# Kernel tuning notes

Measured on AMD Instinct MI355X. Metric: run time of the kernel, lower is better.

Reference implementation:

```python
import jax, jax.numpy as jnp
import numpy as np

B, T, D = 2, 2048, 1024
NH = 16
HD = D // NH


def setup_inputs() -> dict:
    key = jax.random.key(0)
    ks = jax.random.split(key, 5)
    s = 0.02
    return {
        "x": jax.random.normal(ks[0], (B, T, D), dtype=jnp.float32),
        "Wq": jax.random.normal(ks[1], (D, D), dtype=jnp.float32) * s,
        "Wk": jax.random.normal(ks[2], (D, D), dtype=jnp.float32) * s,
        "Wv": jax.random.normal(ks[3], (D, D), dtype=jnp.float32) * s,
        "Wo": jax.random.normal(ks[4], (D, D), dtype=jnp.float32) * s,
        "bo": jnp.zeros((D,), dtype=jnp.float32),
    }


def reference(x, Wq, Wk, Wv, Wo, bo):
    b, t, _ = x.shape
    scale = HD ** -0.5
    # torch Linear: y = x @ W^T
    q = (x @ Wq.T).reshape(b, t, NH, HD)
    k = (x @ Wk.T).reshape(b, t, NH, HD)
    v = (x @ Wv.T).reshape(b, t, NH, HD)
    # scores: [b, nh, t, t]
    s = jnp.einsum("bqhd,bkhd->bhqk", q, k) * scale
    causal = jnp.tril(jnp.ones((t, t), dtype=bool))
    s = jnp.where(causal, s, -jnp.inf)
    p = jax.nn.softmax(s, axis=-1)
    o = jnp.einsum("bhqk,bkhd->bqhd", p, v).reshape(b, t, D)
    return o @ Wo.T + bo
```

## Files before the change

### kernel.cpp

```cpp
#include <hip/hip_runtime.h>


typedef __bf16 bf16x8 __attribute__((ext_vector_type(8)));
typedef float f32x4 __attribute__((ext_vector_type(4)));
typedef unsigned short ushortx8 __attribute__((ext_vector_type(8)));
typedef unsigned short ushortx4 __attribute__((ext_vector_type(4)));

#define T_SEQ 2048
#define NHEAD 16
#define HDIM 64
#define DMODEL 1024

__device__ inline unsigned short f2bf(float f) {
  unsigned int u = __builtin_bit_cast(unsigned int, f);
  unsigned int r = (u + 0x7fffu + ((u >> 16) & 1u)) >> 16;
  return (unsigned short)r;
}

__device__ inline void gl16(const unsigned short* g, unsigned short* l) {
  __builtin_amdgcn_global_load_lds(
      (const __attribute__((address_space(1))) unsigned int*)g,
      (__attribute__((address_space(3))) unsigned int*)l, 16, 0, 0);
}

__global__ void cast_all(const float* __restrict__ x, const float* __restrict__ w0,
                         const float* __restrict__ w1, const float* __restrict__ w2,
                         const float* __restrict__ w3, unsigned short* __restrict__ out) {
  const int NX = 2 * T_SEQ * DMODEL;
  int i = (blockIdx.x * 256 + threadIdx.x) * 4;
  const float* src;
  int off;
  if (i < NX) {
    src = x; off = i;
  } else {
    const int j = i - NX;
    const int sel = j >> 20;
    off = j & ((1 << 20) - 1);
    src = sel == 0 ? w0 : sel == 1 ? w1 : sel == 2 ? w2 : w3;
  }
  float4 v = *reinterpret_cast<const float4*>(src + off);
  ushortx4 o;
  o[0] = f2bf(v.x); o[1] = f2bf(v.y); o[2] = f2bf(v.z); o[3] = f2bf(v.w);
  *reinterpret_cast<ushortx4*>(out + i) = o;
}

__device__ __forceinline__ void gemm_core(
    const unsigned short* __restrict__ A, const unsigned short* __restrict__ Bw,
    int K, int m0, int n0, f32x4 acc[4][4]) {
  __shared__ unsigned short As[4096];
  __shared__ unsigned short Bs[4096];
  const int tid = threadIdx.x;
  const int lane = tid & 63, wid = tid >> 6;
  const int wr = wid >> 1, wc = wid & 1;
  const int lr = lane & 15, lg = lane >> 4;
  const int srow = tid >> 2;
  const int scs = ((tid & 3) ^ (srow & 3)) * 8;
  const unsigned short* ga0 = A + (size_t)(m0 + srow) * K + scs;
  const unsigned short* gb0 = Bw + (size_t)(n0 + srow) * K + scs;
  unsigned short* la0 = As + tid * 8;
  unsigned short* lb0 = Bs + tid * 8;
  const int rca = (lg ^ (lr & 3)) * 8;

  for (int k0 = 0; k0 < K; k0 += 32) {
    __syncthreads();
    gl16(ga0 + k0, la0);
    gl16(ga0 + (size_t)64 * K + k0, la0 + 2048);
    gl16(gb0 + k0, lb0);
    gl16(gb0 + (size_t)64 * K + k0, lb0 + 2048);
    __syncthreads();

    bf16x8 af[4], bfr[4];
#pragma unroll
    for (int t = 0; t < 4; ++t) {
      af[t]  = *reinterpret_cast<const bf16x8*>(&As[(wr * 64 + t * 16 + lr) * 32 + rca]);
      bfr[t] = *reinterpret_cast<const bf16x8*>(&Bs[(wc * 64 + t * 16 + lr) * 32 + rca]);
    }
#pragma unroll
    for (int mi = 0; mi < 4; ++mi)
#pragma unroll
      for (int ni = 0; ni < 4; ++ni)
        acc[mi][ni] = __builtin_amdgcn_mfma_f32_16x16x32_bf16(af[mi], bfr[ni], acc[mi][ni], 0, 0, 0);
  }
}

__global__ __launch_bounds__(256) void gemm_qkv(
    const unsigned short* __restrict__ xb, const unsigned short* __restrict__ Wall,
    unsigned short* __restrict__ Qb, unsigned short* __restrict__ Kb,
    unsigned short* __restrict__ Vtb) {
  const int z = blockIdx.y;
  const int bid = blockIdx.x;
  int m0, n0;
  const unsigned short* A;
  const unsigned short* Bw;
  if (z < 2) {
    n0 = (bid & 7) * 128; m0 = (bid >> 3) * 128;
    A = xb; Bw = Wall + (size_t)z * (DMODEL * DMODEL);
  } else {
    m0 = (bid & 7) * 128; n0 = (bid >> 3) * 128;
    A = Wall + (size_t)2 * (DMODEL * DMODEL); Bw = xb;
  }
  f32x4 acc[4][4] = {};
  gemm_core(A, Bw, DMODEL, m0, n0, acc);

  const int tid = threadIdx.x, lane = tid & 63, wid = tid >> 6;
  const int wr = wid >> 1, wc = wid & 1, lr = lane & 15, lg = lane >> 4;
  const int mb = m0 + wr * 64, nb = n0 + wc * 64;
  const float scale = z == 0 ? 0.125f * 1.44269504089f : 1.0f;
#pragma unroll
  for (int mi = 0; mi < 4; ++mi)
#pragma unroll
    for (int ni = 0; ni < 4; ++ni) {
      const int col = nb + ni * 16 + lr;
#pragma unroll
      for (int j = 0; j < 4; ++j) {
        const int row = mb + mi * 16 + lg * 4 + j;
        const float v = acc[mi][ni][j] * scale;
        if (z < 2) {
          const int b = row >> 11, t = row & (T_SEQ - 1);
          const int h = col >> 6, d = col & (HDIM - 1);
          unsigned short* out = z == 0 ? Qb : Kb;
          out[(((size_t)(b * NHEAD + h) * T_SEQ + t) << 6) + d] = f2bf(v);
        } else {
          const int h = row >> 6, d = row & (HDIM - 1);
          const int b = col >> 11, t = col & (T_SEQ - 1);
          Vtb[(((size_t)(b * NHEAD + h) * HDIM + d) << 11) + t] = f2bf(v);
        }
      }
    }
}

__global__ __launch_bounds__(256) void gemm_proj(
    const unsigned short* __restrict__ Ob, const unsigned short* __restrict__ Wob,
    float* __restrict__ out, const float* __restrict__ bias) {
  const int m0 = blockIdx.y * 128, n0 = blockIdx.x * 128;
  f32x4 acc[4][4] = {};
  gemm_core(Ob, Wob, DMODEL, m0, n0, acc);

  const int tid = threadIdx.x, lane = tid & 63, wid = tid >> 6;
  const int wr = wid >> 1, wc = wid & 1, lr = lane & 15, lg = lane >> 4;
  const int mb = m0 + wr * 64, nb = n0 + wc * 64;
#pragma unroll
  for (int mi = 0; mi < 4; ++mi)
#pragma unroll
    for (int ni = 0; ni < 4; ++ni) {
      const int col = nb + ni * 16 + lr;
      const float bv = bias[col];
#pragma unroll
      for (int j = 0; j < 4; ++j) {
        const int row = mb + mi * 16 + lg * 4 + j;
        out[(size_t)row * DMODEL + col] = acc[mi][ni][j] + bv;
      }
    }
}

__device__ __forceinline__ void attn_step(
    const unsigned short* Kslot, const unsigned short* Vslot,
    const int kh0, const int kh1, const int (&vo)[2][2],
    const bf16x8 (&qf)[2], f32x4 (&acc)[4], float& mrun, float& lrun,
    const bool domask, const int kb, const int q, const int lg) {
  f32x4 s[4] = {};
  __builtin_amdgcn_s_setprio(1);
#pragma unroll
  for (int c = 0; c < 4; ++c) {
    bf16x8 k0 = *reinterpret_cast<const bf16x8*>(&Kslot[kh0 + c * 1024]);
    bf16x8 k1 = *reinterpret_cast<const bf16x8*>(&Kslot[kh1 + c * 1024]);
    s[c] = __builtin_amdgcn_mfma_f32_16x16x32_bf16(k0, qf[0], s[c], 0, 0, 0);
    s[c] = __builtin_amdgcn_mfma_f32_16x16x32_bf16(k1, qf[1], s[c], 0, 0, 0);
  }
  __builtin_amdgcn_s_setprio(0);
  if (domask) {
#pragma unroll
    for (int c = 0; c < 4; ++c)
#pragma unroll
      for (int j = 0; j < 4; ++j) {
        const int k = kb + c * 16 + lg * 4 + j;
        if (k > q) s[c][j] = -INFINITY;
      }
  }
  float tm = -INFINITY;
#pragma unroll
  for (int c = 0; c < 4; ++c)
#pragma unroll
    for (int j = 0; j < 4; ++j) tm = fmaxf(tm, s[c][j]);
  tm = fmaxf(tm, __shfl_xor(tm, 16, 64));
  tm = fmaxf(tm, __shfl_xor(tm, 32, 64));
  if (!__all(tm <= mrun + 8.f)) {
    const float mnew = fmaxf(mrun, tm);
    const float fac = exp2f(mrun - mnew);
    lrun *= fac;
#pragma unroll
    for (int dt = 0; dt < 4; ++dt)
#pragma unroll
      for (int j = 0; j < 4; ++j) acc[dt][j] *= fac;
    mrun = mnew;
  }
  float tsum = 0.f;
#pragma unroll
  for (int c = 0; c < 4; ++c)
#pragma unroll
    for (int j = 0; j < 4; ++j) {
      const float p = exp2f(s[c][j] - mrun);
      s[c][j] = p;
      tsum += p;
    }
  tsum += __shfl_xor(tsum, 16, 64);
  tsum += __shfl_xor(tsum, 32, 64);
  lrun += tsum;

  bf16x8 pb[2];
#pragma unroll
  for (int ks = 0; ks < 2; ++ks) {
    bf16x8 t8;
#pragma unroll
    for (int e = 0; e < 8; ++e) t8[e] = (__bf16)s[ks * 2 + (e >> 2)][e & 3];
    pb[ks] = t8;
  }
  __builtin_amdgcn_s_setprio(1);
#pragma unroll
  for (int dt = 0; dt < 4; ++dt) {
#pragma unroll
    for (int ks = 0; ks < 2; ++ks) {
      uint2 vlo = *reinterpret_cast<const uint2*>(&Vslot[vo[ks][0] + dt * 1024]);
      uint2 vhi = *reinterpret_cast<const uint2*>(&Vslot[vo[ks][1] + dt * 1024]);
      uint4 u;
      u.x = vlo.x; u.y = vlo.y; u.z = vhi.x; u.w = vhi.y;
      bf16x8 vf = __builtin_bit_cast(bf16x8, u);
      acc[dt] = __builtin_amdgcn_mfma_f32_16x16x32_bf16(vf, pb[ks], acc[dt], 0, 0, 0);
    }
  }
  __builtin_amdgcn_s_setprio(0);
}

__global__ __launch_bounds__(512, 4) void flash_attn(
    const unsigned short* __restrict__ Q, const unsigned short* __restrict__ Kg,
    const unsigned short* __restrict__ Vt, unsigned short* __restrict__ O) {
  __shared__ unsigned short Ks[5][4096];
  __shared__ unsigned short Vs[5][4096];
  const int tid = threadIdx.x, lane = tid & 63, wid = tid >> 6;
  const int lr = lane & 15, lg = lane >> 4, wq = wid & 3;
  const int bid = blockIdx.x;
  const int bh = (bid & 7) * 4 + ((bid >> 3) & 3);
  const int a = (bid >> 5) & 15;
  const int b = 31 - a;
  const bool g0 = wid < 4;
  const int myq1 = g0 ? a : b;
  const int q1 = myq1 * 64 + wq * 16 + lr;
  const int q2 = b * 64 + wq * 16 + lr;
  const size_t base = (size_t)bh * (T_SEQ * HDIM);

  bf16x8 qf1[2], qf2[2];
#pragma unroll
  for (int h = 0; h < 2; ++h) {
    qf1[h] = *reinterpret_cast<const bf16x8*>(Q + base + (size_t)q1 * HDIM + h * 32 + lg * 8);
    qf2[h] = *reinterpret_cast<const bf16x8*>(Q + base + (size_t)q2 * HDIM + h * 32 + lg * 8);
  }

  const int srow = tid >> 3;
  const int schk = ((tid & 7) ^ (srow & 7)) * 8;
  const unsigned short* kst = Kg + base + (size_t)srow * HDIM + schk;
  const unsigned short* vst = Vt + base + (size_t)srow * T_SEQ + schk;

#define STAGE(slot, kt_)                                \
  do {                                                  \
    const int kb_ = (kt_) * 64;                         \
    gl16(kst + (size_t)kb_ * HDIM, &Ks[slot][tid * 8]); \
    gl16(vst + kb_, &Vs[slot][tid * 8]);                \
  } while (0)

  const int kh0 = lr * 64 + (((0 * 4 + lg) ^ (lr & 7)) * 8);
  const int kh1 = lr * 64 + (((1 * 4 + lg) ^ (lr & 7)) * 8);
  int vo[2][2];
#pragma unroll
  for (int ks = 0; ks < 2; ++ks) {
    vo[ks][0] = lr * 64 + (((ks * 4 + (lg >> 1)) ^ (lr & 7)) * 8) + (lg & 1) * 4;
    vo[ks][1] = lr * 64 + (((ks * 4 + 2 + (lg >> 1)) ^ (lr & 7)) * 8) + (lg & 1) * 4;
  }

  float m1 = -INFINITY, l1 = 0.f, m2 = -INFINITY, l2 = 0.f;
  f32x4 acc1[4] = {}, acc2[4] = {};

  STAGE(0, 0);
  STAGE(1, 1);
  asm volatile("s_waitcnt vmcnt(2)" ::: "memory");
  __builtin_amdgcn_s_barrier();
  asm volatile("" ::: "memory");

  int sl = 0;
  for (int kt = 0; kt <= a; ++kt) {
    const int st = kt + 2;
    int sst = sl + 2; if (sst >= 5) sst -= 5;
    if (st <= b) STAGE(sst, st);
    attn_step(Ks[sl], Vs[sl], kh0, kh1, vo, qf1, acc1, m1, l1,
              g0 && (kt == a), kt * 64, q1, lg);
    if (kt < a && st <= b) {
      asm volatile("s_waitcnt vmcnt(2)" ::: "memory");
    } else {
      asm volatile("s_waitcnt vmcnt(0)" ::: "memory");
    }
    __builtin_amdgcn_s_barrier();
    asm volatile("" ::: "memory");
    ++sl; if (sl >= 5) sl -= 5;
  }

  {
    int s3 = sl + 2; if (s3 >= 5) s3 -= 5;
    if (a + 3 <= b) STAGE(s3, a + 3);
  }
  for (int t0 = a + 1; t0 <= b; t0 += 2) {
    int s1 = sl + 1; if (s1 >= 5) s1 -= 5;
    int s3 = sl + 3; if (s3 >= 5) s3 -= 5;
    int s4 = sl + 4; if (s4 >= 5) s4 -= 5;
    if (t0 + 3 <= b) STAGE(s3, t0 + 3);
    if (t0 + 4 <= b) STAGE(s4, t0 + 4);
    if (!g0) {
      attn_step(Ks[sl], Vs[sl], kh0, kh1, vo, qf2, acc1, m1, l1,
                t0 == b, t0 * 64, q2, lg);
    } else if (t0 + 1 <= b) {
      attn_step(Ks[s1], Vs[s1], kh0, kh1, vo, qf2, acc2, m2, l2,
                false, (t0 + 1) * 64, q2, lg);
    }
    if (t0 + 4 <= b) {
      asm volatile("s_waitcnt vmcnt(2)" ::: "memory");
    } else {
      asm volatile("s_waitcnt vmcnt(0)" ::: "memory");
    }
    __builtin_amdgcn_s_barrier();
    asm volatile("" ::: "memory");
    sl += 2; if (sl >= 5) sl -= 5;
  }
#undef STAGE

  float* sm = reinterpret_cast<float*>(&Ks[0][0]);
  const int lid = (wq * 64 + lane) * 18;
  if (g0) {
    float* p = sm + lid;
    p[0] = m2; p[1] = l2;
#pragma unroll
    for (int dt = 0; dt < 4; ++dt)
#pragma unroll
      for (int j = 0; j < 4; ++j) p[2 + dt * 4 + j] = acc2[dt][j];
  }
  __syncthreads();
  if (!g0) {
    const float* p = sm + lid;
    const float mo = p[0], lo = p[1];
    const float ms = fmaxf(m1, mo);
    const float f1 = exp2f(m1 - ms), f2 = exp2f(mo - ms);
    l1 = l1 * f1 + lo * f2;
#pragma unroll
    for (int dt = 0; dt < 4; ++dt)
#pragma unroll
      for (int j = 0; j < 4; ++j)
        acc1[dt][j] = acc1[dt][j] * f1 + p[2 + dt * 4 + j] * f2;
  }

  const int b_ = bh >> 4, h_ = bh & (NHEAD - 1);
  const float inv = 1.0f / l1;
  unsigned short* orow = O + (((size_t)(b_ * T_SEQ + q1)) << 10) + h_ * HDIM + lg * 4;
#pragma unroll
  for (int dt = 0; dt < 4; ++dt) {
    ushortx4 o4;
#pragma unroll
    for (int j = 0; j < 4; ++j) o4[j] = f2bf(acc1[dt][j] * inv);
    *reinterpret_cast<ushortx4*>(orow + dt * 16) = o4;
  }
}

extern "C" void kernel_launch(void* const* d_in, const int* in_sizes, int n_in,
                              void* d_out, int out_size, void* d_ws, size_t ws_size,
                              hipStream_t stream) {
  const float* x  = (const float*)d_in[0];
  const float* Wq = (const float*)d_in[1];
  const float* Wk = (const float*)d_in[2];
  const float* Wv = (const float*)d_in[3];
  const float* Wo = (const float*)d_in[4];
  const float* bo = (const float*)d_in[5];
  float* out = (float*)d_out;

  const int M = 2 * T_SEQ;
  const int NXD = DMODEL * DMODEL;
  const int NX = M * DMODEL;

  unsigned short* ws = (unsigned short*)d_ws;
  unsigned short* xb  = ws;
  unsigned short* Wqb = xb + NX;
  unsigned short* Wob = Wqb + 3 * (size_t)NXD;
  unsigned short* Qb  = Wqb + 4 * (size_t)NXD;
  unsigned short* Kbf = Qb + NX;
  unsigned short* Vtb = Kbf + NX;
  unsigned short* Ob  = Vtb + NX;

  cast_all<<<(NX + 4 * NXD) / 1024, 256, 0, stream>>>(x, Wq, Wk, Wv, Wo, xb);

  dim3 gq(256, 3);
  gemm_qkv<<<gq, 256, 0, stream>>>(xb, Wqb, Qb, Kbf, Vtb);

  flash_attn<<<512, 512, 0, stream>>>(Qb, Kbf, Vtb, Ob);

  dim3 gg(DMODEL / 128, M / 128);
  gemm_proj<<<gg, 256, 0, stream>>>(Ob, Wob, out, bo);
}
```

Measured before the change: 113.2 us.

## Permute V layout for single 16-byte LDS reads, defer row-sum reduction, narrow proj tiles

The QKV GEMM epilogue now writes V^T with a permuted token order within each 32-token group. The attention kernel can then load each V fragment as one 16-byte LDS read instead of two 8-byte reads stitched together. The per-step cross-lane shuffle reduction of the softmax row sum moves to a single reduction after the loop. The output projection GEMM switches to 128x64 tiles, doubling the block count to improve occupancy and load balance on the many-CU device, at the cost of less B-tile reuse per block.

New measurement: 104.1 us. -8.1%, faster.

```diff
diff --git a/kernel.cpp b/kernel.cpp
--- a/kernel.cpp
+++ b/kernel.cpp
@@ -83,6 +83,45 @@
   }
 }
 
+__device__ __forceinline__ void gemm_core_n64(
+    const unsigned short* __restrict__ A, const unsigned short* __restrict__ Bw,
+    int K, int m0, int n0, f32x4 acc[4][2]) {
+  __shared__ unsigned short As[4096];
+  __shared__ unsigned short Bs[2048];
+  const int tid = threadIdx.x;
+  const int lane = tid & 63, wid = tid >> 6;
+  const int wr = wid >> 1, wc = wid & 1;
+  const int lr = lane & 15, lg = lane >> 4;
+  const int srow = tid >> 2;
+  const int scs = ((tid & 3) ^ (srow & 3)) * 8;
+  const unsigned short* ga0 = A + (size_t)(m0 + srow) * K + scs;
+  const unsigned short* gb0 = Bw + (size_t)(n0 + srow) * K + scs;
+  unsigned short* la0 = As + tid * 8;
+  unsigned short* lb0 = Bs + tid * 8;
+  const int rca = (lg ^ (lr & 3)) * 8;
+
+  for (int k0 = 0; k0 < K; k0 += 32) {
+    __syncthreads();
+    gl16(ga0 + k0, la0);
+    gl16(ga0 + (size_t)64 * K + k0, la0 + 2048);
+    gl16(gb0 + k0, lb0);
+    __syncthreads();
+
+    bf16x8 af[4], bfr[2];
+#pragma unroll
+    for (int t = 0; t < 4; ++t)
+      af[t] = *reinterpret_cast<const bf16x8*>(&As[(wr * 64 + t * 16 + lr) * 32 + rca]);
+#pragma unroll
+    for (int t = 0; t < 2; ++t)
+      bfr[t] = *reinterpret_cast<const bf16x8*>(&Bs[(wc * 32 + t * 16 + lr) * 32 + rca]);
+#pragma unroll
+    for (int mi = 0; mi < 4; ++mi)
+#pragma unroll
+      for (int ni = 0; ni < 2; ++ni)
+        acc[mi][ni] = __builtin_amdgcn_mfma_f32_16x16x32_bf16(af[mi], bfr[ni], acc[mi][ni], 0, 0, 0);
+  }
+}
+
 __global__ __launch_bounds__(256) void gemm_qkv(
     const unsigned short* __restrict__ xb, const unsigned short* __restrict__ Wall,
     unsigned short* __restrict__ Qb, unsigned short* __restrict__ Kb,
@@ -122,8 +161,11 @@
           out[(((size_t)(b * NHEAD + h) * T_SEQ + t) << 6) + d] = f2bf(v);
         } else {
           const int h = row >> 6, d = row & (HDIM - 1);
-          const int b = col >> 11, t = col & (T_SEQ - 1);
-          Vtb[(((size_t)(b * NHEAD + h) * HDIM + d) << 11) + t] = f2bf(v);
+          const int b = col >> 11, tt = col & (T_SEQ - 1);
+          const int nib = (tt >> 2) & 7;
+          const int nib2 = ((nib & 3) << 1) | (nib >> 2);
+          const int tp = (tt & ~31) | (nib2 << 2) | (tt & 3);
+          Vtb[(((size_t)(b * NHEAD + h) * HDIM + d) << 11) + tp] = f2bf(v);
         }
       }
     }
@@ -132,17 +174,17 @@
 __global__ __launch_bounds__(256) void gemm_proj(
     const unsigned short* __restrict__ Ob, const unsigned short* __restrict__ Wob,
     float* __restrict__ out, const float* __restrict__ bias) {
-  const int m0 = blockIdx.y * 128, n0 = blockIdx.x * 128;
-  f32x4 acc[4][4] = {};
-  gemm_core(Ob, Wob, DMODEL, m0, n0, acc);
+  const int m0 = blockIdx.y * 128, n0 = blockIdx.x * 64;
+  f32x4 acc[4][2] = {};
+  gemm_core_n64(Ob, Wob, DMODEL, m0, n0, acc);
 
   const int tid = threadIdx.x, lane = tid & 63, wid = tid >> 6;
   const int wr = wid >> 1, wc = wid & 1, lr = lane & 15, lg = lane >> 4;
-  const int mb = m0 + wr * 64, nb = n0 + wc * 64;
+  const int mb = m0 + wr * 64, nb = n0 + wc * 32;
 #pragma unroll
   for (int mi = 0; mi < 4; ++mi)
 #pragma unroll
-    for (int ni = 0; ni < 4; ++ni) {
+    for (int ni = 0; ni < 2; ++ni) {
       const int col = nb + ni * 16 + lr;
       const float bv = bias[col];
 #pragma unroll
@@ -155,7 +197,7 @@
 
 __device__ __forceinline__ void attn_step(
     const unsigned short* Kslot, const unsigned short* Vslot,
-    const int kh0, const int kh1, const int (&vo)[2][2],
+    const int kh0, const int kh1, const int (&vo)[2],
     const bf16x8 (&qf)[2], f32x4 (&acc)[4], float& mrun, float& lrun,
     const bool domask, const int kb, const int q, const int lg) {
   f32x4 s[4] = {};
@@ -203,8 +245,6 @@
       s[c][j] = p;
       tsum += p;
     }
-  tsum += __shfl_xor(tsum, 16, 64);
-  tsum += __shfl_xor(tsum, 32, 64);
   lrun += tsum;
 
   bf16x8 pb[2];
@@ -220,11 +260,7 @@
   for (int dt = 0; dt < 4; ++dt) {
 #pragma unroll
     for (int ks = 0; ks < 2; ++ks) {
-      uint2 vlo = *reinterpret_cast<const uint2*>(&Vslot[vo[ks][0] + dt * 1024]);
-      uint2 vhi = *reinterpret_cast<const uint2*>(&Vslot[vo[ks][1] + dt * 1024]);
-      uint4 u;
-      u.x = vlo.x; u.y = vlo.y; u.z = vhi.x; u.w = vhi.y;
-      bf16x8 vf = __builtin_bit_cast(bf16x8, u);
+      bf16x8 vf = *reinterpret_cast<const bf16x8*>(&Vslot[vo[ks] + dt * 1024]);
       acc[dt] = __builtin_amdgcn_mfma_f32_16x16x32_bf16(vf, pb[ks], acc[dt], 0, 0, 0);
     }
   }
@@ -267,14 +303,12 @@
     gl16(vst + kb_, &Vs[slot][tid * 8]);                \
   } while (0)
 
-  const int kh0 = lr * 64 + (((0 * 4 + lg) ^ (lr & 7)) * 8);
-  const int kh1 = lr * 64 + (((1 * 4 + lg) ^ (lr & 7)) * 8);
-  int vo[2][2];
-#pragma unroll
-  for (int ks = 0; ks < 2; ++ks) {
-    vo[ks][0] = lr * 64 + (((ks * 4 + (lg >> 1)) ^ (lr & 7)) * 8) + (lg & 1) * 4;
-    vo[ks][1] = lr * 64 + (((ks * 4 + 2 + (lg >> 1)) ^ (lr & 7)) * 8) + (lg & 1) * 4;
-  }
+  const int kh0 = lr * 64 + ((lg ^ (lr & 7)) * 8);
+  const int kh1 = lr * 64 + (((4 + lg) ^ (lr & 7)) * 8);
+  int vo[2];
+#pragma unroll
+  for (int ks = 0; ks < 2; ++ks)
+    vo[ks] = lr * 64 + (((ks * 4 + lg) ^ (lr & 7)) * 8);
 
   float m1 = -INFINITY, l1 = 0.f, m2 = -INFINITY, l2 = 0.f;
   f32x4 acc1[4] = {}, acc2[4] = {};
@@ -354,6 +388,9 @@
         acc1[dt][j] = acc1[dt][j] * f1 + p[2 + dt * 4 + j] * f2;
   }
 
+  l1 += __shfl_xor(l1, 16, 64);
+  l1 += __shfl_xor(l1, 32, 64);
+
   const int b_ = bh >> 4, h_ = bh & (NHEAD - 1);
   const float inv = 1.0f / l1;
   unsigned short* orow = O + (((size_t)(b_ * T_SEQ + q1)) << 10) + h_ * HDIM + lg * 4;
@@ -397,6 +434,6 @@
 
   flash_attn<<<512, 512, 0, stream>>>(Qb, Kbf, Vtb, Ob);
 
-  dim3 gg(DMODEL / 128, M / 128);
+  dim3 gg(DMODEL / 64, M / 128);
   gemm_proj<<<gg, 256, 0, stream>>>(Ob, Wob, out, bo);
 }
```
